# Performance work log

Measured on AMD Instinct MI355X. Metric: run time of the kernel, lower is better.

Reference implementation:

```python
import jax, jax.numpy as jnp
import numpy as np

N = 100000   # num nodes
E = 600000   # num edges
H = 128      # hidden dim
R = 8        # num relations
B = 4        # num bases


def setup_inputs() -> dict:
    key = jax.random.key(0)
    ks = jax.random.split(key, 12)
    return {
        "node_ids": jnp.arange(N, dtype=jnp.int64 if jax.config.jax_enable_x64 else jnp.int32),
        "src": jax.random.randint(ks[0], (E,), 0, N),
        "dst": jax.random.randint(ks[1], (E,), 0, N),
        "etype": jax.random.randint(ks[2], (E,), 0, R),
        "embedding": jax.random.normal(ks[3], (N, H), dtype=jnp.float32),
        "V1": jax.random.normal(ks[4], (B, H, H), dtype=jnp.float32) * 0.05,
        "comp1": jax.random.normal(ks[5], (R, B), dtype=jnp.float32),
        "loop1": jax.random.normal(ks[6], (H, H), dtype=jnp.float32) * 0.05,
        "bias1": jax.random.normal(ks[7], (H,), dtype=jnp.float32) * 0.05,
        "V2": jax.random.normal(ks[8], (B, H, H), dtype=jnp.float32) * 0.05,
        "comp2": jax.random.normal(ks[9], (R, B), dtype=jnp.float32),
        "loop2": jax.random.normal(ks[10], (H, H), dtype=jnp.float32) * 0.05,
        "bias2": jax.random.normal(ks[11], (H,), dtype=jnp.float32) * 0.05,
    }


def _rgcn_layer(h, src, dst, etype, V, comp, loopW, bias, activate):
    # basis decomposition: W_r = sum_b comp[r,b] * V[b]   -> [R, in, out]
    W = jnp.einsum('rb,bio->rio', comp, V)
    # transform all nodes under all relations once (avoids per-edge GEMM): [N, R, out]
    hw = jnp.einsum('ni,rio->nro', h, W)
    # gather per-edge message for its (src, relation): [E, out]
    m = hw[src, etype]
    # scatter-sum aggregation at destination nodes
    agg = jax.ops.segment_sum(m, dst, num_segments=h.shape[0])
    out = agg + bias + h @ loopW  # bias + self-loop
    return jax.nn.relu(out) if activate else out


def reference(node_ids, src, dst, etype, embedding,
              V1, comp1, loop1, bias1,
              V2, comp2, loop2, bias2):
    h = embedding[node_ids]                       # EmbeddingLayer
    h = _rgcn_layer(h, src, dst, etype, V1, comp1, loop1, bias1, activate=True)
    h = _rgcn_layer(h, src, dst, etype, V2, comp2, loop2, bias2, activate=False)
    return h
```

## Files before the change

### kernel.cpp

```cpp
#include <hip/hip_runtime.h>
#include <hip/hip_bf16.h>

#define NN 100000
#define NE 600000
#define HH 128
#define NB 4
#define TILE 2048
#define NTILES ((NN + TILE - 1) / TILE)

typedef __attribute__((ext_vector_type(8))) short bf16x8;
typedef __attribute__((ext_vector_type(4))) float f32x4;
typedef __attribute__((ext_vector_type(4))) float vfloat4;
typedef __attribute__((ext_vector_type(4))) unsigned short ushort4v;

static __device__ __forceinline__ short f2bf(float f) {
  unsigned u = __float_as_uint(f);
  unsigned r = (u + 0x7fffu + ((u >> 16) & 1u)) >> 16;
  return (short)r;
}

static __device__ __forceinline__ float bf2f(short s) {
  unsigned u = (unsigned)(unsigned short)s;
  return __uint_as_float(u << 16);
}

__global__ __launch_bounds__(256) void build_wt(const float* __restrict__ V,
                                                const float* __restrict__ loopW,
                                                short* __restrict__ W8)
{
  int idx = blockIdx.x * blockDim.x + threadIdx.x;
  int j  = idx & 7;
  int o  = (idx >> 3) & 127;
  int kb = idx >> 10;
  int k  = kb * 8 + j;
  float v;
  if (k < 512) v = V[(size_t)k * HH + o];
  else         v = loopW[(size_t)(k - 512) * HH + o];
  W8[idx] = f2bf(v);
}

__global__ __launch_bounds__(256) void cast_h(const float* __restrict__ in,
                                              short* __restrict__ out)
{
  const int n8 = NN * HH / 8;
  for (int i = blockIdx.x * blockDim.x + threadIdx.x; i < n8; i += gridDim.x * blockDim.x) {
    const vfloat4* p = reinterpret_cast<const vfloat4*>(in + i * 8);
    vfloat4 a = p[0], b = p[1];
    bf16x8 o;
#pragma unroll
    for (int j = 0; j < 4; ++j) { o[j] = f2bf(a[j]); o[j + 4] = f2bf(b[j]); }
    reinterpret_cast<bf16x8*>(out)[i] = o;
  }
}


__global__ __launch_bounds__(256) void hist_deg(const int* __restrict__ dst,
                                                int* __restrict__ deg)
{
  int e = blockIdx.x * blockDim.x + threadIdx.x;
  if (e < NE) atomicAdd(&deg[dst[e]], 1);
}

__global__ __launch_bounds__(256) void scan_tiles(const int* __restrict__ deg,
                                                  int* __restrict__ tilesum)
{
  __shared__ int red[256];
  const int tid = threadIdx.x;
  int base = blockIdx.x * TILE + tid * 8;
  int s = 0;
#pragma unroll
  for (int j = 0; j < 8; ++j) {
    int i = base + j;
    if (i < NN) s += deg[i];
  }
  red[tid] = s;
  __syncthreads();
  for (int off = 128; off > 0; off >>= 1) {
    if (tid < off) red[tid] += red[tid + off];
    __syncthreads();
  }
  if (tid == 0) tilesum[blockIdx.x] = red[0];
}

__global__ __launch_bounds__(256) void scan_final(const int* deg,
                                                  const int* __restrict__ tilesum,
                                                  int* __restrict__ rowptr,
                                                  int* cursor)
{
  __shared__ int lds[256];
  const int tid = threadIdx.x;
  int pre = 0;
  for (int t = 0; t < NTILES; ++t)
    if (t < blockIdx.x) pre += tilesum[t];

  int base = blockIdx.x * TILE + tid * 8;
  int d[8];
  int s = 0;
#pragma unroll
  for (int j = 0; j < 8; ++j) {
    int i = base + j;
    d[j] = (i < NN) ? deg[i] : 0;
    s += d[j];
  }
  lds[tid] = s;
  __syncthreads();
  for (int off = 1; off < 256; off <<= 1) {
    int t = (tid >= off) ? lds[tid - off] : 0;
    __syncthreads();
    lds[tid] += t;
    __syncthreads();
  }
  int run = pre + lds[tid] - s;
#pragma unroll
  for (int j = 0; j < 8; ++j) {
    int i = base + j;
    if (i < NN) {
      rowptr[i] = run;
      cursor[i] = run;
      run += d[j];
    }
  }
  if (blockIdx.x == NTILES - 1 && tid == 255)
    rowptr[NN] = pre + lds[255];
}

__global__ __launch_bounds__(256) void scatter_edges(
    const int* __restrict__ src, const int* __restrict__ dst, const int* __restrict__ ety,
    int* __restrict__ cursor, int* __restrict__ csr)
{
  int e = blockIdx.x * blockDim.x + threadIdx.x;
  if (e >= NE) return;
  int d = dst[e];
  int p = atomicAdd(&cursor[d], 1);
  csr[p] = src[e] | (ety[e] << 20);
}

__global__ __launch_bounds__(256) void gather_g(
    const int* __restrict__ rowptr, const int* __restrict__ csr,
    const float* __restrict__ comp,
    const short* __restrict__ hbf,
    short* __restrict__ g)
{
  int wid = (int)(blockIdx.x * 4 + (threadIdx.x >> 6));
  wid = __builtin_amdgcn_readfirstlane(wid);
  if (wid >= NN) return;
  const int lane = threadIdx.x & 63;
  const int b = lane >> 4;
  const int q = lane & 15;

  const int start = rowptr[wid];
  const int end = rowptr[wid + 1];

  float acc[8] = {0.f, 0.f, 0.f, 0.f, 0.f, 0.f, 0.f, 0.f};
  int i = start;
  for (; i + 2 <= end; i += 2) {
    int e0 = csr[i], e1 = csr[i + 1];
    const bf16x8* p0 = reinterpret_cast<const bf16x8*>(hbf + (size_t)(e0 & 0xFFFFF) * HH);
    const bf16x8* p1 = reinterpret_cast<const bf16x8*>(hbf + (size_t)(e1 & 0xFFFFF) * HH);
    bf16x8 h0 = p0[q];
    bf16x8 h1 = p1[q];
    float c0 = comp[(e0 >> 20) * NB + b];
    float c1 = comp[(e1 >> 20) * NB + b];
#pragma unroll
    for (int j = 0; j < 8; ++j) acc[j] += bf2f(h0[j]) * c0;
#pragma unroll
    for (int j = 0; j < 8; ++j) acc[j] += bf2f(h1[j]) * c1;
  }
  if (i < end) {
    int e0 = csr[i];
    const bf16x8* p0 = reinterpret_cast<const bf16x8*>(hbf + (size_t)(e0 & 0xFFFFF) * HH);
    bf16x8 h0 = p0[q];
    float c0 = comp[(e0 >> 20) * NB + b];
#pragma unroll
    for (int j = 0; j < 8; ++j) acc[j] += bf2f(h0[j]) * c0;
  }

  bf16x8 o;
#pragma unroll
  for (int j = 0; j < 8; ++j) o[j] = f2bf(acc[j]);
  reinterpret_cast<bf16x8*>(g + (size_t)wid * 512)[lane] = o;
}

template<int FINAL>
__global__ __launch_bounds__(256) void gemm_out(
    const short* __restrict__ g,
    const short* __restrict__ hbf,
    const short* __restrict__ W8,
    const float* __restrict__ bias,
    short* __restrict__ outH,
    float* __restrict__ outF)
{
  __shared__ bf16x8 wlds[2][512];

  const int tid  = threadIdx.x;
  const int wave = tid >> 6;
  const int lane = tid & 63;
  const int t0 = blockIdx.x * 128 + wave * 16;
  const int t1 = t0 + 64;
  const bool valid0 = (t0 < NN);
  const bool valid1 = (t1 < NN);
  const int r  = lane & 15;
  const int g8 = lane >> 4;

  const size_t row0 = valid0 ? (size_t)(t0 + r) : 0;
  const size_t row1 = valid1 ? (size_t)(t1 + r) : 0;
  const bf16x8* ga0 = reinterpret_cast<const bf16x8*>(g + row0 * 512);
  const bf16x8* ga1 = reinterpret_cast<const bf16x8*>(g + row1 * 512);
  const bf16x8* ha0 = reinterpret_cast<const bf16x8*>(hbf + row0 * HH);
  const bf16x8* ha1 = reinterpret_cast<const bf16x8*>(hbf + row1 * HH);
  const bf16x8* wsrc = reinterpret_cast<const bf16x8*>(W8);

  f32x4 acc0[8], acc1[8];
#pragma unroll
  for (int ct = 0; ct < 8; ++ct) {
    acc0[ct] = (f32x4){0.f, 0.f, 0.f, 0.f};
    acc1[ct] = (f32x4){0.f, 0.f, 0.f, 0.f};
  }

  wlds[0][tid]       = wsrc[tid];
  wlds[0][tid + 256] = wsrc[tid + 256];
  __syncthreads();

#pragma unroll 1
  for (int ks = 0; ks < 20; ++ks) {
    const int cur = ks & 1;
    if (ks < 19) {
      bf16x8 n0 = wsrc[(ks + 1) * 512 + tid];
      bf16x8 n1 = wsrc[(ks + 1) * 512 + 256 + tid];
      wlds[cur ^ 1][tid]       = n0;
      wlds[cur ^ 1][tid + 256] = n1;
    }
    bf16x8 a0 = (ks < 16) ? ga0[ks * 4 + g8] : ha0[(ks - 16) * 4 + g8];
    bf16x8 a1 = (ks < 16) ? ga1[ks * 4 + g8] : ha1[(ks - 16) * 4 + g8];
#pragma unroll
    for (int ct = 0; ct < 8; ++ct) {
      bf16x8 w = wlds[cur][g8 * 128 + ct * 16 + r];
      acc0[ct] = __builtin_amdgcn_mfma_f32_16x16x32_bf16(w, a0, acc0[ct], 0, 0, 0);
      acc1[ct] = __builtin_amdgcn_mfma_f32_16x16x32_bf16(w, a1, acc1[ct], 0, 0, 0);
    }
    __syncthreads();
  }

#pragma unroll
  for (int ct = 0; ct < 8; ++ct) {
    const int o = ct * 16 + g8 * 4;
    vfloat4 bs = *reinterpret_cast<const vfloat4*>(bias + o);
    if (FINAL) {
      vfloat4 x0, x1;
#pragma unroll
      for (int rr = 0; rr < 4; ++rr) { x0[rr] = acc0[ct][rr] + bs[rr]; x1[rr] = acc1[ct][rr] + bs[rr]; }
      if (valid0) reinterpret_cast<vfloat4*>(outF + (size_t)(t0 + r) * HH)[ct * 4 + g8] = x0;
      if (valid1) reinterpret_cast<vfloat4*>(outF + (size_t)(t1 + r) * HH)[ct * 4 + g8] = x1;
    } else {
      ushort4v s0, s1;
#pragma unroll
      for (int rr = 0; rr < 4; ++rr) {
        s0[rr] = (unsigned short)f2bf(fmaxf(acc0[ct][rr] + bs[rr], 0.f));
        s1[rr] = (unsigned short)f2bf(fmaxf(acc1[ct][rr] + bs[rr], 0.f));
      }
      if (valid0) reinterpret_cast<ushort4v*>(outH + (size_t)(t0 + r) * HH)[ct * 4 + g8] = s0;
      if (valid1) reinterpret_cast<ushort4v*>(outH + (size_t)(t1 + r) * HH)[ct * 4 + g8] = s1;
    }
  }
}

extern "C" void kernel_launch(void* const* d_in, const int* in_sizes, int n_in,
                              void* d_out, int out_size, void* d_ws, size_t ws_size,
                              hipStream_t stream)
{
  const int*   srcp  = (const int*)d_in[1];
  const int*   dstp  = (const int*)d_in[2];
  const int*   etp   = (const int*)d_in[3];
  const float* emb   = (const float*)d_in[4];
  const float* V1    = (const float*)d_in[5];
  const float* comp1 = (const float*)d_in[6];
  const float* loop1 = (const float*)d_in[7];
  const float* bias1 = (const float*)d_in[8];
  const float* V2    = (const float*)d_in[9];
  const float* comp2 = (const float*)d_in[10];
  const float* loop2 = (const float*)d_in[11];
  const float* bias2 = (const float*)d_in[12];
  float* out = (float*)d_out;

  char* ws = (char*)d_ws;
  short* Wt1     = (short*)(ws);
  short* Wt2     = (short*)(ws + 163840);
  short* hbf1    = (short*)(ws + 327680);
  short* hbf2    = (short*)(ws + 25927680);
  short* g       = (short*)(ws + 51527680);
  int*   deg     = (int*)  (ws + 153927680);
  int*   rowptr  = (int*)  (ws + 154327680);
  int*   csr     = (int*)  (ws + 154727696);
  int*   tilesum = (int*)  (ws + 157127696);

  const int gemm_blocks = (NN + 127) / 128;
  const int agg_blocks  = (NN + 3) / 4;
  const int e_blocks    = (NE + 255) / 256;

  hipMemsetAsync(deg, 0, NN * sizeof(int), stream);
  hipLaunchKernelGGL(hist_deg, dim3(e_blocks), dim3(256), 0, stream, dstp, deg);
  hipLaunchKernelGGL(scan_tiles, dim3(NTILES), dim3(256), 0, stream, deg, tilesum);
  hipLaunchKernelGGL(scan_final, dim3(NTILES), dim3(256), 0, stream,
                     deg, tilesum, rowptr, deg);
  hipLaunchKernelGGL(scatter_edges, dim3(e_blocks), dim3(256), 0, stream,
                     srcp, dstp, etp, deg, csr);

  hipLaunchKernelGGL(build_wt, dim3(320), dim3(256), 0, stream, V1, loop1, Wt1);
  hipLaunchKernelGGL(build_wt, dim3(320), dim3(256), 0, stream, V2, loop2, Wt2);
  hipLaunchKernelGGL(cast_h, dim3(2048), dim3(256), 0, stream, emb, hbf1);

  hipLaunchKernelGGL(gather_g, dim3(agg_blocks), dim3(256), 0, stream,
                     rowptr, csr, comp1, hbf1, g);
  hipLaunchKernelGGL((gemm_out<0>), dim3(gemm_blocks), dim3(256), 0, stream,
                     g, hbf1, Wt1, bias1, hbf2, (float*)nullptr);

  hipLaunchKernelGGL(gather_g, dim3(agg_blocks), dim3(256), 0, stream,
                     rowptr, csr, comp2, hbf2, g);
  hipLaunchKernelGGL((gemm_out<1>), dim3(gemm_blocks), dim3(256), 0, stream,
                     g, hbf2, Wt2, bias2, (short*)nullptr, out);
}
```

Baseline: 295.4 us.

## Fuse edge gather and basis GEMM into one per-layer kernel via LDS staging

Merges the per-node gather of basis-weighted neighbor features and the MFMA GEMM into a single kernel per layer. The gathered rows (64 nodes × 512 bf16) are kept in a swizzled LDS tile instead of going through a global intermediate, which removes that buffer's write and read-back. The gather loop is also unrolled to four edges at a time. In exchange, each block handles 64 nodes instead of 128, and a wave processes its 16 nodes serially before the GEMM starts. The large LDS footprint may also limit occupancy.

Measured after the change: 495.2 us. 67.6% more time.

```diff
diff --git a/kernel.cpp b/kernel.cpp
--- a/kernel.cpp
+++ b/kernel.cpp
@@ -135,91 +135,87 @@
   csr[p] = src[e] | (ety[e] << 20);
 }
 
-__global__ __launch_bounds__(256) void gather_g(
+template<int FINAL>
+__global__ __launch_bounds__(256, 2) void rgcn_layer(
     const int* __restrict__ rowptr, const int* __restrict__ csr,
     const float* __restrict__ comp,
-    const short* __restrict__ hbf,
-    short* __restrict__ g)
-{
-  int wid = (int)(blockIdx.x * 4 + (threadIdx.x >> 6));
-  wid = __builtin_amdgcn_readfirstlane(wid);
-  if (wid >= NN) return;
-  const int lane = threadIdx.x & 63;
-  const int b = lane >> 4;
-  const int q = lane & 15;
-
-  const int start = rowptr[wid];
-  const int end = rowptr[wid + 1];
-
-  float acc[8] = {0.f, 0.f, 0.f, 0.f, 0.f, 0.f, 0.f, 0.f};
-  int i = start;
-  for (; i + 2 <= end; i += 2) {
-    int e0 = csr[i], e1 = csr[i + 1];
-    const bf16x8* p0 = reinterpret_cast<const bf16x8*>(hbf + (size_t)(e0 & 0xFFFFF) * HH);
-    const bf16x8* p1 = reinterpret_cast<const bf16x8*>(hbf + (size_t)(e1 & 0xFFFFF) * HH);
-    bf16x8 h0 = p0[q];
-    bf16x8 h1 = p1[q];
-    float c0 = comp[(e0 >> 20) * NB + b];
-    float c1 = comp[(e1 >> 20) * NB + b];
-#pragma unroll
-    for (int j = 0; j < 8; ++j) acc[j] += bf2f(h0[j]) * c0;
-#pragma unroll
-    for (int j = 0; j < 8; ++j) acc[j] += bf2f(h1[j]) * c1;
-  }
-  if (i < end) {
-    int e0 = csr[i];
-    const bf16x8* p0 = reinterpret_cast<const bf16x8*>(hbf + (size_t)(e0 & 0xFFFFF) * HH);
-    bf16x8 h0 = p0[q];
-    float c0 = comp[(e0 >> 20) * NB + b];
-#pragma unroll
-    for (int j = 0; j < 8; ++j) acc[j] += bf2f(h0[j]) * c0;
-  }
-
-  bf16x8 o;
-#pragma unroll
-  for (int j = 0; j < 8; ++j) o[j] = f2bf(acc[j]);
-  reinterpret_cast<bf16x8*>(g + (size_t)wid * 512)[lane] = o;
-}
-
-template<int FINAL>
-__global__ __launch_bounds__(256) void gemm_out(
-    const short* __restrict__ g,
     const short* __restrict__ hbf,
     const short* __restrict__ W8,
     const float* __restrict__ bias,
     short* __restrict__ outH,
     float* __restrict__ outF)
 {
-  __shared__ bf16x8 wlds[2][512];
+  __shared__ bf16x8 gl[64][64];
+  __shared__ bf16x8 wl[2][512];
 
   const int tid  = threadIdx.x;
   const int wave = tid >> 6;
   const int lane = tid & 63;
-  const int t0 = blockIdx.x * 128 + wave * 16;
-  const int t1 = t0 + 64;
-  const bool valid0 = (t0 < NN);
-  const bool valid1 = (t1 < NN);
-  const int r  = lane & 15;
-  const int g8 = lane >> 4;
-
-  const size_t row0 = valid0 ? (size_t)(t0 + r) : 0;
-  const size_t row1 = valid1 ? (size_t)(t1 + r) : 0;
-  const bf16x8* ga0 = reinterpret_cast<const bf16x8*>(g + row0 * 512);
-  const bf16x8* ga1 = reinterpret_cast<const bf16x8*>(g + row1 * 512);
-  const bf16x8* ha0 = reinterpret_cast<const bf16x8*>(hbf + row0 * HH);
-  const bf16x8* ha1 = reinterpret_cast<const bf16x8*>(hbf + row1 * HH);
+  const int b  = lane >> 4;
+  const int q  = lane & 15;
+  const int base = blockIdx.x * 64;
+
+  const int myrow  = wave * 16 + q;
+  const int mynode = base + myrow;
+  const bool myvalid = (mynode < NN);
+  const bf16x8* ha = reinterpret_cast<const bf16x8*>(hbf + (size_t)(myvalid ? mynode : 0) * HH);
+  bf16x8 hreg[4];
+#pragma unroll
+  for (int j = 0; j < 4; ++j) hreg[j] = ha[j * 4 + b];
+
+#pragma unroll 1
+  for (int nn = 0; nn < 16; ++nn) {
+    const int row = wave * 16 + nn;
+    const int node = base + row;
+    int start = 0, end = 0;
+    if (node < NN) { start = rowptr[node]; end = rowptr[node + 1]; }
+
+    float acc[8] = {0.f, 0.f, 0.f, 0.f, 0.f, 0.f, 0.f, 0.f};
+    int i = start;
+    for (; i + 4 <= end; i += 4) {
+      int e0 = csr[i], e1 = csr[i + 1], e2 = csr[i + 2], e3 = csr[i + 3];
+      bf16x8 h0 = reinterpret_cast<const bf16x8*>(hbf + (size_t)(e0 & 0xFFFFF) * HH)[q];
+      bf16x8 h1 = reinterpret_cast<const bf16x8*>(hbf + (size_t)(e1 & 0xFFFFF) * HH)[q];
+      bf16x8 h2 = reinterpret_cast<const bf16x8*>(hbf + (size_t)(e2 & 0xFFFFF) * HH)[q];
+      bf16x8 h3 = reinterpret_cast<const bf16x8*>(hbf + (size_t)(e3 & 0xFFFFF) * HH)[q];
+      float c0 = comp[(e0 >> 20) * NB + b];
+      float c1 = comp[(e1 >> 20) * NB + b];
+      float c2 = comp[(e2 >> 20) * NB + b];
+      float c3 = comp[(e3 >> 20) * NB + b];
+#pragma unroll
+      for (int j = 0; j < 8; ++j) acc[j] += bf2f(h0[j]) * c0;
+#pragma unroll
+      for (int j = 0; j < 8; ++j) acc[j] += bf2f(h1[j]) * c1;
+#pragma unroll
+      for (int j = 0; j < 8; ++j) acc[j] += bf2f(h2[j]) * c2;
+#pragma unroll
+      for (int j = 0; j < 8; ++j) acc[j] += bf2f(h3[j]) * c3;
+    }
+    for (; i < end; ++i) {
+      int e0 = csr[i];
+      bf16x8 h0 = reinterpret_cast<const bf16x8*>(hbf + (size_t)(e0 & 0xFFFFF) * HH)[q];
+      float c0 = comp[(e0 >> 20) * NB + b];
+#pragma unroll
+      for (int j = 0; j < 8; ++j) acc[j] += bf2f(h0[j]) * c0;
+    }
+
+    bf16x8 o;
+#pragma unroll
+    for (int j = 0; j < 8; ++j) o[j] = f2bf(acc[j]);
+    gl[row][lane ^ (nn & 7)] = o;
+  }
+
   const bf16x8* wsrc = reinterpret_cast<const bf16x8*>(W8);
-
-  f32x4 acc0[8], acc1[8];
-#pragma unroll
-  for (int ct = 0; ct < 8; ++ct) {
-    acc0[ct] = (f32x4){0.f, 0.f, 0.f, 0.f};
-    acc1[ct] = (f32x4){0.f, 0.f, 0.f, 0.f};
-  }
-
-  wlds[0][tid]       = wsrc[tid];
-  wlds[0][tid + 256] = wsrc[tid + 256];
+  wl[0][tid]       = wsrc[tid];
+  wl[0][tid + 256] = wsrc[tid + 256];
   __syncthreads();
+
+  const int r  = q;
+  const int g8 = b;
+
+  f32x4 acc[8];
+#pragma unroll
+  for (int ct = 0; ct < 8; ++ct) acc[ct] = (f32x4){0.f, 0.f, 0.f, 0.f};
 
 #pragma unroll 1
   for (int ks = 0; ks < 20; ++ks) {
@@ -227,16 +223,14 @@
     if (ks < 19) {
       bf16x8 n0 = wsrc[(ks + 1) * 512 + tid];
       bf16x8 n1 = wsrc[(ks + 1) * 512 + 256 + tid];
-      wlds[cur ^ 1][tid]       = n0;
-      wlds[cur ^ 1][tid + 256] = n1;
-    }
-    bf16x8 a0 = (ks < 16) ? ga0[ks * 4 + g8] : ha0[(ks - 16) * 4 + g8];
-    bf16x8 a1 = (ks < 16) ? ga1[ks * 4 + g8] : ha1[(ks - 16) * 4 + g8];
+      wl[cur ^ 1][tid]       = n0;
+      wl[cur ^ 1][tid + 256] = n1;
+    }
+    bf16x8 a = (ks < 16) ? gl[myrow][(ks * 4 + g8) ^ (r & 7)] : hreg[ks - 16];
 #pragma unroll
     for (int ct = 0; ct < 8; ++ct) {
-      bf16x8 w = wlds[cur][g8 * 128 + ct * 16 + r];
-      acc0[ct] = __builtin_amdgcn_mfma_f32_16x16x32_bf16(w, a0, acc0[ct], 0, 0, 0);
-      acc1[ct] = __builtin_amdgcn_mfma_f32_16x16x32_bf16(w, a1, acc1[ct], 0, 0, 0);
+      bf16x8 w = wl[cur][g8 * 128 + ct * 16 + r];
+      acc[ct] = __builtin_amdgcn_mfma_f32_16x16x32_bf16(w, a, acc[ct], 0, 0, 0);
     }
     __syncthreads();
   }
@@ -246,20 +240,16 @@
     const int o = ct * 16 + g8 * 4;
     vfloat4 bs = *reinterpret_cast<const vfloat4*>(bias + o);
     if (FINAL) {
-      vfloat4 x0, x1;
-#pragma unroll
-      for (int rr = 0; rr < 4; ++rr) { x0[rr] = acc0[ct][rr] + bs[rr]; x1[rr] = acc1[ct][rr] + bs[rr]; }
-      if (valid0) reinterpret_cast<vfloat4*>(outF + (size_t)(t0 + r) * HH)[ct * 4 + g8] = x0;
-      if (valid1) reinterpret_cast<vfloat4*>(outF + (size_t)(t1 + r) * HH)[ct * 4 + g8] = x1;
+      vfloat4 x;
+#pragma unroll
+      for (int rr = 0; rr < 4; ++rr) x[rr] = acc[ct][rr] + bs[rr];
+      if (myvalid) reinterpret_cast<vfloat4*>(outF + (size_t)mynode * HH)[ct * 4 + g8] = x;
     } else {
-      ushort4v s0, s1;
-#pragma unroll
-      for (int rr = 0; rr < 4; ++rr) {
-        s0[rr] = (unsigned short)f2bf(fmaxf(acc0[ct][rr] + bs[rr], 0.f));
-        s1[rr] = (unsigned short)f2bf(fmaxf(acc1[ct][rr] + bs[rr], 0.f));
-      }
-      if (valid0) reinterpret_cast<ushort4v*>(outH + (size_t)(t0 + r) * HH)[ct * 4 + g8] = s0;
-      if (valid1) reinterpret_cast<ushort4v*>(outH + (size_t)(t1 + r) * HH)[ct * 4 + g8] = s1;
+      ushort4v s;
+#pragma unroll
+      for (int rr = 0; rr < 4; ++rr)
+        s[rr] = (unsigned short)f2bf(fmaxf(acc[ct][rr] + bs[rr], 0.f));
+      if (myvalid) reinterpret_cast<ushort4v*>(outH + (size_t)mynode * HH)[ct * 4 + g8] = s;
     }
   }
 }
@@ -287,15 +277,13 @@
   short* Wt2     = (short*)(ws + 163840);
   short* hbf1    = (short*)(ws + 327680);
   short* hbf2    = (short*)(ws + 25927680);
-  short* g       = (short*)(ws + 51527680);
-  int*   deg     = (int*)  (ws + 153927680);
-  int*   rowptr  = (int*)  (ws + 154327680);
-  int*   csr     = (int*)  (ws + 154727696);
-  int*   tilesum = (int*)  (ws + 157127696);
-
-  const int gemm_blocks = (NN + 127) / 128;
-  const int agg_blocks  = (NN + 3) / 4;
-  const int e_blocks    = (NE + 255) / 256;
+  int*   deg     = (int*)  (ws + 51527680);
+  int*   rowptr  = (int*)  (ws + 51927680);
+  int*   csr     = (int*)  (ws + 52327696);
+  int*   tilesum = (int*)  (ws + 54727696);
+
+  const int layer_blocks = (NN + 63) / 64;
+  const int e_blocks     = (NE + 255) / 256;
 
   hipMemsetAsync(deg, 0, NN * sizeof(int), stream);
   hipLaunchKernelGGL(hist_deg, dim3(e_blocks), dim3(256), 0, stream, dstp, deg);
@@ -309,13 +297,9 @@
   hipLaunchKernelGGL(build_wt, dim3(320), dim3(256), 0, stream, V2, loop2, Wt2);
   hipLaunchKernelGGL(cast_h, dim3(2048), dim3(256), 0, stream, emb, hbf1);
 
-  hipLaunchKernelGGL(gather_g, dim3(agg_blocks), dim3(256), 0, stream,
-                     rowptr, csr, comp1, hbf1, g);
-  hipLaunchKernelGGL((gemm_out<0>), dim3(gemm_blocks), dim3(256), 0, stream,
-                     g, hbf1, Wt1, bias1, hbf2, (float*)nullptr);
-
-  hipLaunchKernelGGL(gather_g, dim3(agg_blocks), dim3(256), 0, stream,
-                     rowptr, csr, comp2, hbf2, g);
-  hipLaunchKernelGGL((gemm_out<1>), dim3(gemm_blocks), dim3(256), 0, stream,
-                     g, hbf2, Wt2, bias2, (short*)nullptr, out);
-}
+  hipLaunchKernelGGL((rgcn_layer<0>), dim3(layer_blocks), dim3(256), 0, stream,
+                     rowptr, csr, comp1, hbf1, Wt1, bias1, hbf2, (float*)nullptr);
+
+  hipLaunchKernelGGL((rgcn_layer<1>), dim3(layer_blocks), dim3(256), 0, stream,
+                     rowptr, csr, comp2, hbf2, Wt2, bias2, (short*)nullptr, out);
+}
```
